# Performance work log

Hardware: AMD Instinct MI355X
Metric: run time of the kernel (lower is better)

Reference implementation:

```python
import jax, jax.numpy as jnp
import numpy as np

B = 32            # decode batch (N flat tokens, q_len=1 each)
D_MODEL = 4096
H = 32            # query heads
HKV = 8           # kv heads (GQA)
HD = 128          # head dim
KVLEN = 2048      # context length per sequence
BLOCK = 256       # paged-cache block size
NBPS = KVLEN // BLOCK          # blocks per sequence = 8
NBLOCKS = B * NBPS             # 256
NSLOTS = NBLOCKS * BLOCK       # 65536
EPS = 1e-6
THETA = 10000.0
NEG = -1e30


def setup_inputs() -> dict:
    key = jax.random.key(0)
    ks = jax.random.split(key, 8)
    seqs = jax.random.normal(ks[0], (B, D_MODEL), dtype=jnp.float32)
    Wq = jax.random.normal(ks[1], (D_MODEL, H * HD), dtype=jnp.float32) * 0.02
    Wk = jax.random.normal(ks[2], (D_MODEL, HKV * HD), dtype=jnp.float32) * 0.02
    Wv = jax.random.normal(ks[3], (D_MODEL, HKV * HD), dtype=jnp.float32) * 0.02
    Wo = jax.random.normal(ks[4], (H * HD, D_MODEL), dtype=jnp.float32) * 0.02
    qn_w = jnp.ones((HD,), dtype=jnp.float32)
    kn_w = jnp.ones((HD,), dtype=jnp.float32)
    k_cache = jax.random.normal(ks[5], (NSLOTS, HKV, HD), dtype=jnp.float32) * 0.02
    v_cache = jax.random.normal(ks[6], (NSLOTS, HKV, HD), dtype=jnp.float32) * 0.02
    # decode step: each seq owns NBPS contiguous blocks; new token goes to last slot
    input_pos = jnp.full((B,), KVLEN - 1, dtype=jnp.int32)
    slot_mapping = (jnp.arange(B, dtype=jnp.int32) * NBPS * BLOCK + (KVLEN - 1)).astype(jnp.int32)
    block_tables = jnp.arange(NBLOCKS, dtype=jnp.int32).reshape(B, NBPS)
    context_lens = jnp.full((B,), KVLEN, dtype=jnp.int32)
    return {
        'seqs': seqs, 'Wq': Wq, 'Wk': Wk, 'Wv': Wv, 'Wo': Wo,
        'qn_w': qn_w, 'kn_w': kn_w, 'k_cache': k_cache, 'v_cache': v_cache,
        'input_pos': input_pos, 'slot_mapping': slot_mapping,
        'block_tables': block_tables, 'context_lens': context_lens,
    }


def _rmsnorm(x, w):
    return x * jax.lax.rsqrt(jnp.mean(x * x, axis=-1, keepdims=True) + EPS) * w


def _rope(x, pos):
    # x: [N, heads, HD], pos: [N]
    half = HD // 2
    inv = 1.0 / (THETA ** (jnp.arange(half, dtype=jnp.float32) / half))
    ang = pos.astype(jnp.float32)[:, None] * inv          # [N, half]
    cos = jnp.cos(ang)[:, None, :]
    sin = jnp.sin(ang)[:, None, :]
    x1, x2 = x[..., :half], x[..., half:]
    return jnp.concatenate([x1 * cos - x2 * sin, x2 * cos + x1 * sin], axis=-1)


def reference(seqs, Wq, Wk, Wv, Wo, qn_w, kn_w, k_cache, v_cache,
              input_pos, slot_mapping, block_tables, context_lens):
    # QKV projections (flat token layout, N = B decode tokens)
    q = (seqs @ Wq).reshape(B, H, HD)
    k = (seqs @ Wk).reshape(B, HKV, HD)
    v = (seqs @ Wv).reshape(B, HKV, HD)
    # qk-norm then RoPE
    q = _rmsnorm(q, qn_w)
    k = _rmsnorm(k, kn_w)
    q = _rope(q, input_pos)
    k = _rope(k, input_pos)
    # paged KV-cache store (slot_mapping scatter)
    kc = k_cache.at[slot_mapping].set(k)
    vc = v_cache.at[slot_mapping].set(v)
    # block-table-indexed gather: slots per sequence [B, KVLEN]
    slots = (block_tables[:, :, None] * BLOCK
             + jnp.arange(BLOCK, dtype=jnp.int32)[None, None, :]).reshape(B, -1)
    K = kc[slots]   # [B, L, HKV, HD]
    V = vc[slots]   # [B, L, HKV, HD]
    L = slots.shape[1]
    # GQA attention: group query heads over kv heads
    G = H // HKV
    qg = q.reshape(B, HKV, G, HD)
    scale = 1.0 / jnp.sqrt(jnp.float32(HD))
    scores = jnp.einsum('bkgd,blkd->bkgl', qg, K) * scale   # [B, HKV, G, L]
    valid = jnp.arange(L, dtype=jnp.int32)[None, :] < context_lens[:, None]
    scores = jnp.where(valid[:, None, None, :], scores, NEG)
    p = jax.nn.softmax(scores, axis=-1)
    out = jnp.einsum('bkgl,blkd->bkgd', p, V).reshape(B, H * HD)
    return out @ Wo
```

## Files before the change

kernel.cpp:

```cpp
#include <hip/hip_runtime.h>
#include <hip/hip_bf16.h>
#include <math.h>

#define B_     32
#define DM_    4096
#define H_     32
#define HKV_   8
#define G_     4
#define HD_    128
#define KVLEN_ 2048
#define NBPS_  8
#define NQKV_  6144
#define KSPLIT_ 16
#define KC_    256
#define ASPLIT_ 16
#define APOS_  128

__global__ __launch_bounds__(256) void qkv_gemm(
    const float* __restrict__ seqs, const float* __restrict__ Wq,
    const float* __restrict__ Wk, const float* __restrict__ Wv,
    float* __restrict__ P1) {
  const int tid = threadIdx.x;
  const int nid = blockIdx.x % 24;
  const int kid = blockIdx.x / 24;
  const int k0 = kid * KC_;

  __shared__ __align__(16) float sT[KC_ * 36];
  #pragma unroll
  for (int m = 0; m < 32; ++m)
    sT[tid * 36 + m] = seqs[m * DM_ + k0 + tid];
  __syncthreads();

  const int ct = tid & 127;
  const int mh = tid >> 7;
  const int n  = nid * 256 + ct * 2;

  const float* W; int col, ldw;
  if (nid < 16)      { W = Wq; col = n;        ldw = 4096; }
  else if (nid < 20) { W = Wk; col = n - 4096; ldw = 1024; }
  else               { W = Wv; col = n - 5120; ldw = 1024; }

  float2 acc[16];
  #pragma unroll
  for (int r = 0; r < 16; ++r) acc[r] = make_float2(0.f, 0.f);

  const float2* wp = (const float2*)(W + (size_t)k0 * ldw + col);
  const int ldw2 = ldw >> 1;

  #pragma unroll 4
  for (int kk = 0; kk < KC_; ++kk) {
    float2 w = wp[(size_t)kk * ldw2];
    const float4* s4 = (const float4*)(sT + kk * 36 + mh * 16);
    #pragma unroll
    for (int rq = 0; rq < 4; ++rq) {
      float4 a = s4[rq];
      acc[rq*4+0].x = fmaf(a.x, w.x, acc[rq*4+0].x);
      acc[rq*4+0].y = fmaf(a.x, w.y, acc[rq*4+0].y);
      acc[rq*4+1].x = fmaf(a.y, w.x, acc[rq*4+1].x);
      acc[rq*4+1].y = fmaf(a.y, w.y, acc[rq*4+1].y);
      acc[rq*4+2].x = fmaf(a.z, w.x, acc[rq*4+2].x);
      acc[rq*4+2].y = fmaf(a.z, w.y, acc[rq*4+2].y);
      acc[rq*4+3].x = fmaf(a.w, w.x, acc[rq*4+3].x);
      acc[rq*4+3].y = fmaf(a.w, w.y, acc[rq*4+3].y);
    }
  }

  float* o = P1 + (size_t)kid * 32 * NQKV_ + n;
  #pragma unroll
  for (int r = 0; r < 16; ++r) {
    int m = mh * 16 + r;
    *(float2*)(o + (size_t)m * NQKV_) = acc[r];
  }
}

__global__ __launch_bounds__(128) void reduce_norm_rope(
    const float* __restrict__ P1, const float* __restrict__ qn_w,
    const float* __restrict__ kn_w, const int* __restrict__ input_pos,
    float* __restrict__ qf, float* __restrict__ knew, float* __restrict__ vnew) {
  const int b = blockIdx.x / 48;
  const int hh = blockIdx.x % 48;
  const int tid = threadIdx.x;

  int col0, kind;
  if (hh < 32)      { kind = 0; col0 = hh * 128; }
  else if (hh < 40) { kind = 1; col0 = 4096 + (hh - 32) * 128; }
  else              { kind = 2; col0 = 5120 + (hh - 40) * 128; }

  float x = 0.f;
  const float* p = P1 + (size_t)b * NQKV_ + col0 + tid;
  #pragma unroll
  for (int s = 0; s < KSPLIT_; ++s) x += p[(size_t)s * 32 * NQKV_];

  if (kind == 2) {
    vnew[(size_t)b * 1024 + (hh - 40) * 128 + tid] = x;
    return;
  }

  __shared__ float lds[128];
  __shared__ float wred[2];
  float ss = x * x;
  #pragma unroll
  for (int off = 32; off > 0; off >>= 1) ss += __shfl_down(ss, off);
  if ((tid & 63) == 0) wred[tid >> 6] = ss;
  __syncthreads();
  float tot = wred[0] + wred[1];
  float r = rsqrtf(tot * (1.f / 128.f) + 1e-6f);
  const float* wv = (kind == 0) ? qn_w : kn_w;
  x = x * r * wv[tid];

  lds[tid] = x;
  __syncthreads();

  if (tid < 64) {
    float pos = (float)input_pos[b];
    float inv = powf(10000.f, -(float)tid * (1.f / 64.f));
    float ang = pos * inv;
    float c = cosf(ang), s = sinf(ang);
    float x1 = lds[tid], x2 = lds[tid + 64];
    float o1 = x1 * c - x2 * s;
    float o2 = x2 * c + x1 * s;
    float* dst = (kind == 0) ? (qf + (size_t)b * 4096 + hh * 128)
                             : (knew + (size_t)b * 1024 + (hh - 32) * 128);
    dst[tid] = o1;
    dst[tid + 64] = o2;
  }
}

__global__ __launch_bounds__(512) void attn_decode(
    const float* __restrict__ qf, const float* __restrict__ knew,
    const float* __restrict__ vnew, const float* __restrict__ kc,
    const float* __restrict__ vc, const int* __restrict__ block_tables,
    const int* __restrict__ slot_mapping, const int* __restrict__ context_lens,
    float* __restrict__ pacc, float* __restrict__ pls) {
  const int b   = blockIdx.x >> 4;
  const int sp  = blockIdx.x & 15;
  const int tid = threadIdx.x;
  const int w   = tid >> 6;
  const int lane = tid & 63;
  const int gi  = lane >> 4;
  const int l16 = lane & 15;
  const int d0  = l16 * 8;

  const int ctx   = context_lens[b];
  const int fslot = slot_mapping[b];
  const int base  = sp * APOS_;

  const int page  = block_tables[b * NBPS_ + (base >> 8)];
  const int slot0 = (page << 8) + (base & 255);

  const float scale = 0.08838834764831845f;
  float q[4][8];
  #pragma unroll
  for (int g = 0; g < 4; ++g) {
    const float4* qp = (const float4*)(qf + ((size_t)b * H_ + w * G_ + g) * HD_ + d0);
    float4 a = qp[0], c = qp[1];
    q[g][0] = a.x * scale; q[g][1] = a.y * scale; q[g][2] = a.z * scale; q[g][3] = a.w * scale;
    q[g][4] = c.x * scale; q[g][5] = c.y * scale; q[g][6] = c.z * scale; q[g][7] = c.w * scale;
  }

  const float* knp = knew + ((size_t)b * HKV_ + w) * HD_ + d0;
  const float* vnp = vnew + ((size_t)b * HKV_ + w) * HD_ + d0;
  const float* kcb = kc + ((size_t)slot0 * HKV_ + w) * HD_ + d0;
  const float* vcb = vc + ((size_t)slot0 * HKV_ + w) * HD_ + d0;

  float ls[4] = {0.f, 0.f, 0.f, 0.f};
  float acc[4][8];
  #pragma unroll
  for (int g = 0; g < 4; ++g)
    #pragma unroll
    for (int j = 0; j < 8; ++j) acc[g][j] = 0.f;

  for (int it = 0; it < APOS_ / 4; ++it) {
    const int off = it * 4 + gi;
    const int pos = base + off;
    if (pos < ctx) {
      const int slot = slot0 + off;
      const float* kp = (slot == fslot) ? knp : (kcb + (size_t)off * (HKV_ * HD_));
      const float* vp = (slot == fslot) ? vnp : (vcb + (size_t)off * (HKV_ * HD_));
      float4 k1 = ((const float4*)kp)[0];
      float4 k2 = ((const float4*)kp)[1];
      float4 v1 = ((const float4*)vp)[0];
      float4 v2 = ((const float4*)vp)[1];
      float kk8[8] = {k1.x, k1.y, k1.z, k1.w, k2.x, k2.y, k2.z, k2.w};
      float vv[8]  = {v1.x, v1.y, v1.z, v1.w, v2.x, v2.y, v2.z, v2.w};

      float s[4];
      #pragma unroll
      for (int g = 0; g < 4; ++g) {
        float t = 0.f;
        #pragma unroll
        for (int j = 0; j < 8; ++j) t = fmaf(q[g][j], kk8[j], t);
        s[g] = t;
      }
      #pragma unroll
      for (int o2 = 1; o2 < 16; o2 <<= 1) {
        #pragma unroll
        for (int g = 0; g < 4; ++g) s[g] += __shfl_xor(s[g], o2);
      }
      #pragma unroll
      for (int g = 0; g < 4; ++g) {
        float pw = __expf(s[g]);
        ls[g] += pw;
        #pragma unroll
        for (int j = 0; j < 8; ++j) acc[g][j] = fmaf(pw, vv[j], acc[g][j]);
      }
    }
  }

  #pragma unroll
  for (int o2 = 16; o2 < 64; o2 <<= 1) {
    #pragma unroll
    for (int g = 0; g < 4; ++g) {
      ls[g] += __shfl_xor(ls[g], o2);
      #pragma unroll
      for (int j = 0; j < 8; ++j) acc[g][j] += __shfl_xor(acc[g][j], o2);
    }
  }

  if (gi == 0) {
    #pragma unroll
    for (int g = 0; g < 4; ++g) {
      float* dst = pacc + (((size_t)sp * B_ + b) * H_ + (w * G_ + g)) * HD_ + d0;
      float4 o1 = {acc[g][0], acc[g][1], acc[g][2], acc[g][3]};
      float4 o2 = {acc[g][4], acc[g][5], acc[g][6], acc[g][7]};
      ((float4*)dst)[0] = o1;
      ((float4*)dst)[1] = o2;
      if (l16 == 0) pls[((size_t)sp * B_ + b) * H_ + (w * G_ + g)] = ls[g];
    }
  }
}

__global__ __launch_bounds__(256) void attn_merge(
    const float* __restrict__ pacc, const float* __restrict__ pls,
    float* __restrict__ attnb) {
  const int idx = blockIdx.x * 256 + threadIdx.x;
  const int bh  = idx >> 5;
  const float4* p4 = (const float4*)pacc;
  float4 A = {0.f, 0.f, 0.f, 0.f};
  float L = 0.f;
  #pragma unroll
  for (int sp = 0; sp < ASPLIT_; ++sp) {
    float4 t = p4[(size_t)sp * 32768 + idx];
    A.x += t.x; A.y += t.y; A.z += t.z; A.w += t.w;
    L += pls[sp * (B_ * H_) + bh];
  }
  float r = 1.f / L;
  A.x *= r; A.y *= r; A.z *= r; A.w *= r;
  ((float4*)attnb)[idx] = A;
}

__global__ __launch_bounds__(256) void oproj_gemm(
    const float* __restrict__ A, const float* __restrict__ Wo,
    float* __restrict__ P2) {
  const int tid = threadIdx.x;
  const int nid = blockIdx.x & 15;
  const int kid = blockIdx.x >> 4;
  const int k0 = kid * KC_;

  __shared__ __align__(16) float sT[KC_ * 36];
  #pragma unroll
  for (int m = 0; m < 32; ++m)
    sT[tid * 36 + m] = A[m * 4096 + k0 + tid];
  __syncthreads();

  const int ct = tid & 127;
  const int mh = tid >> 7;
  const int n  = nid * 256 + ct * 2;

  float2 acc[16];
  #pragma unroll
  for (int r = 0; r < 16; ++r) acc[r] = make_float2(0.f, 0.f);

  const float2* wp = (const float2*)(Wo + (size_t)k0 * 4096 + n);

  #pragma unroll 4
  for (int kk = 0; kk < KC_; ++kk) {
    float2 w = wp[(size_t)kk * 2048];
    const float4* s4 = (const float4*)(sT + kk * 36 + mh * 16);
    #pragma unroll
    for (int rq = 0; rq < 4; ++rq) {
      float4 a = s4[rq];
      acc[rq*4+0].x = fmaf(a.x, w.x, acc[rq*4+0].x);
      acc[rq*4+0].y = fmaf(a.x, w.y, acc[rq*4+0].y);
      acc[rq*4+1].x = fmaf(a.y, w.x, acc[rq*4+1].x);
      acc[rq*4+1].y = fmaf(a.y, w.y, acc[rq*4+1].y);
      acc[rq*4+2].x = fmaf(a.z, w.x, acc[rq*4+2].x);
      acc[rq*4+2].y = fmaf(a.z, w.y, acc[rq*4+2].y);
      acc[rq*4+3].x = fmaf(a.w, w.x, acc[rq*4+3].x);
      acc[rq*4+3].y = fmaf(a.w, w.y, acc[rq*4+3].y);
    }
  }

  float* o = P2 + (size_t)kid * 32 * 4096 + n;
  #pragma unroll
  for (int r = 0; r < 16; ++r) {
    int m = mh * 16 + r;
    *(float2*)(o + (size_t)m * 4096) = acc[r];
  }
}

__global__ __launch_bounds__(256) void oproj_reduce(
    const float* __restrict__ P2, float* __restrict__ out) {
  const int idx = blockIdx.x * 256 + threadIdx.x;
  float s = 0.f;
  #pragma unroll
  for (int t = 0; t < KSPLIT_; ++t) s += P2[(size_t)t * 131072 + idx];
  out[idx] = s;
}

extern "C" void kernel_launch(void* const* d_in, const int* in_sizes, int n_in,
                              void* d_out, int out_size, void* d_ws, size_t ws_size,
                              hipStream_t stream) {
  const float* seqs = (const float*)d_in[0];
  const float* Wq   = (const float*)d_in[1];
  const float* Wk   = (const float*)d_in[2];
  const float* Wv   = (const float*)d_in[3];
  const float* Wo   = (const float*)d_in[4];
  const float* qn_w = (const float*)d_in[5];
  const float* kn_w = (const float*)d_in[6];
  const float* kc   = (const float*)d_in[7];
  const float* vc   = (const float*)d_in[8];
  const int* input_pos = (const int*)d_in[9];
  const int* slot_map  = (const int*)d_in[10];
  const int* btab      = (const int*)d_in[11];
  const int* ctx       = (const int*)d_in[12];
  float* out = (float*)d_out;

  char* w = (char*)d_ws;
  float* P1    = (float*)(w);
  float* qf    = (float*)(w + 12582912);
  float* knew  = (float*)(w + 13107200);
  float* vnew  = (float*)(w + 13238272);
  float* attnb = (float*)(w + 13369344);
  float* pacc  = (float*)(w + 13893632);
  float* pls   = (float*)(w + 22282240);
  float* P2    = (float*)(w + 22347776);

  qkv_gemm<<<24 * KSPLIT_, 256, 0, stream>>>(seqs, Wq, Wk, Wv, P1);
  reduce_norm_rope<<<B_ * 48, 128, 0, stream>>>(P1, qn_w, kn_w, input_pos, qf, knew, vnew);
  attn_decode<<<B_ * ASPLIT_, 512, 0, stream>>>(qf, knew, vnew, kc, vc, btab, slot_map, ctx, pacc, pls);
  attn_merge<<<128, 256, 0, stream>>>(pacc, pls, attnb);
  oproj_gemm<<<16 * KSPLIT_, 256, 0, stream>>>(attnb, Wo, P2);
  oproj_reduce<<<512, 256, 0, stream>>>(P2, out);
}
```

Baseline: 211.8 us.

## Pre-transpose GEMM activations, stream weights nontemporally, add fast path in attention

Adds a small transpose kernel so the QKV and output-projection GEMMs read the activation operand straight from global memory (wave-uniform, cached) instead of staging it through LDS with a barrier. Weight and KV-cache loads become nontemporal, and unrolling is increased. The attention kernel gets a branch-free fast path for splits that hold neither the newly written slot nor a context boundary. The output projection uses 512 threads with 8 rows each to raise occupancy. In exchange it adds two extra kernel launches and workspace for the transposed activations.

```diff
diff --git a/kernel.cpp b/kernel.cpp
--- a/kernel.cpp
+++ b/kernel.cpp
@@ -16,8 +16,30 @@
 #define ASPLIT_ 16
 #define APOS_  128
 
+typedef float vf4 __attribute__((ext_vector_type(4)));
+typedef float vf2 __attribute__((ext_vector_type(2)));
+
+__global__ __launch_bounds__(256) void transpose32(
+    const float* __restrict__ in, float* __restrict__ out) {
+  __shared__ float t[32][65];
+  const int tid = threadIdx.x;
+  const int k0 = blockIdx.x * 64;
+  #pragma unroll
+  for (int it = 0; it < 8; ++it) {
+    int m = it * 4 + (tid >> 6);
+    int k = tid & 63;
+    t[m][k] = in[(size_t)m * DM_ + k0 + k];
+  }
+  __syncthreads();
+  #pragma unroll
+  for (int it = 0; it < 8; ++it) {
+    int flat = it * 256 + tid;
+    out[(size_t)k0 * 32 + flat] = t[flat & 31][flat >> 5];
+  }
+}
+
 __global__ __launch_bounds__(256) void qkv_gemm(
-    const float* __restrict__ seqs, const float* __restrict__ Wq,
+    const float* __restrict__ seqsT, const float* __restrict__ Wq,
     const float* __restrict__ Wk, const float* __restrict__ Wv,
     float* __restrict__ P1) {
   const int tid = threadIdx.x;
@@ -25,14 +47,8 @@
   const int kid = blockIdx.x / 24;
   const int k0 = kid * KC_;
 
-  __shared__ __align__(16) float sT[KC_ * 36];
-  #pragma unroll
-  for (int m = 0; m < 32; ++m)
-    sT[tid * 36 + m] = seqs[m * DM_ + k0 + tid];
-  __syncthreads();
-
   const int ct = tid & 127;
-  const int mh = tid >> 7;
+  const int mh16 = __builtin_amdgcn_readfirstlane((tid >> 7) << 4);
   const int n  = nid * 256 + ct * 2;
 
   const float* W; int col, ldw;
@@ -44,31 +60,30 @@
   #pragma unroll
   for (int r = 0; r < 16; ++r) acc[r] = make_float2(0.f, 0.f);
 
-  const float2* wp = (const float2*)(W + (size_t)k0 * ldw + col);
+  const vf2* wp = (const vf2*)(W + (size_t)k0 * ldw + col);
   const int ldw2 = ldw >> 1;
-
-  #pragma unroll 4
+  const vf4* ap = (const vf4*)(seqsT + (size_t)k0 * 32 + mh16);
+
+  #pragma unroll 8
   for (int kk = 0; kk < KC_; ++kk) {
-    float2 w = wp[(size_t)kk * ldw2];
-    const float4* s4 = (const float4*)(sT + kk * 36 + mh * 16);
-    #pragma unroll
-    for (int rq = 0; rq < 4; ++rq) {
-      float4 a = s4[rq];
-      acc[rq*4+0].x = fmaf(a.x, w.x, acc[rq*4+0].x);
-      acc[rq*4+0].y = fmaf(a.x, w.y, acc[rq*4+0].y);
-      acc[rq*4+1].x = fmaf(a.y, w.x, acc[rq*4+1].x);
-      acc[rq*4+1].y = fmaf(a.y, w.y, acc[rq*4+1].y);
-      acc[rq*4+2].x = fmaf(a.z, w.x, acc[rq*4+2].x);
-      acc[rq*4+2].y = fmaf(a.z, w.y, acc[rq*4+2].y);
-      acc[rq*4+3].x = fmaf(a.w, w.x, acc[rq*4+3].x);
-      acc[rq*4+3].y = fmaf(a.w, w.y, acc[rq*4+3].y);
-    }
+    vf2 w = __builtin_nontemporal_load(wp + (size_t)kk * ldw2);
+    vf4 a0 = ap[kk * 8 + 0];
+    vf4 a1 = ap[kk * 8 + 1];
+    vf4 a2 = ap[kk * 8 + 2];
+    vf4 a3 = ap[kk * 8 + 3];
+    #define FMA2(av, r) \
+      acc[r].x = fmaf(av, w.x, acc[r].x); acc[r].y = fmaf(av, w.y, acc[r].y);
+    FMA2(a0.x, 0)  FMA2(a0.y, 1)  FMA2(a0.z, 2)  FMA2(a0.w, 3)
+    FMA2(a1.x, 4)  FMA2(a1.y, 5)  FMA2(a1.z, 6)  FMA2(a1.w, 7)
+    FMA2(a2.x, 8)  FMA2(a2.y, 9)  FMA2(a2.z, 10) FMA2(a2.w, 11)
+    FMA2(a3.x, 12) FMA2(a3.y, 13) FMA2(a3.z, 14) FMA2(a3.w, 15)
+    #undef FMA2
   }
 
   float* o = P1 + (size_t)kid * 32 * NQKV_ + n;
   #pragma unroll
   for (int r = 0; r < 16; ++r) {
-    int m = mh * 16 + r;
+    int m = mh16 + r;
     *(float2*)(o + (size_t)m * NQKV_) = acc[r];
   }
 }
@@ -147,6 +162,9 @@
 
   const int page  = block_tables[b * NBPS_ + (base >> 8)];
   const int slot0 = (page << 8) + (base & 255);
+  const int rel   = fslot - slot0;
+  const bool hasf = (rel >= 0) && (rel < APOS_);
+  const int nv    = min(APOS_, ctx - base);
 
   const float scale = 0.08838834764831845f;
   float q[4][8];
@@ -170,42 +188,59 @@
     #pragma unroll
     for (int j = 0; j < 8; ++j) acc[g][j] = 0.f;
 
-  for (int it = 0; it < APOS_ / 4; ++it) {
-    const int off = it * 4 + gi;
-    const int pos = base + off;
-    if (pos < ctx) {
-      const int slot = slot0 + off;
-      const float* kp = (slot == fslot) ? knp : (kcb + (size_t)off * (HKV_ * HD_));
-      const float* vp = (slot == fslot) ? vnp : (vcb + (size_t)off * (HKV_ * HD_));
-      float4 k1 = ((const float4*)kp)[0];
-      float4 k2 = ((const float4*)kp)[1];
-      float4 v1 = ((const float4*)vp)[0];
-      float4 v2 = ((const float4*)vp)[1];
-      float kk8[8] = {k1.x, k1.y, k1.z, k1.w, k2.x, k2.y, k2.z, k2.w};
-      float vv[8]  = {v1.x, v1.y, v1.z, v1.w, v2.x, v2.y, v2.z, v2.w};
-
-      float s[4];
-      #pragma unroll
-      for (int g = 0; g < 4; ++g) {
-        float t = 0.f;
-        #pragma unroll
-        for (int j = 0; j < 8; ++j) t = fmaf(q[g][j], kk8[j], t);
-        s[g] = t;
+  #define ATTN_STEP(K1, K2, V1, V2)                                       \
+    {                                                                     \
+      float kk8[8] = {K1.x, K1.y, K1.z, K1.w, K2.x, K2.y, K2.z, K2.w};    \
+      float vv[8]  = {V1.x, V1.y, V1.z, V1.w, V2.x, V2.y, V2.z, V2.w};    \
+      float s[4];                                                         \
+      _Pragma("unroll")                                                   \
+      for (int g = 0; g < 4; ++g) {                                       \
+        float t = 0.f;                                                    \
+        _Pragma("unroll")                                                 \
+        for (int j = 0; j < 8; ++j) t = fmaf(q[g][j], kk8[j], t);         \
+        s[g] = t;                                                         \
+      }                                                                   \
+      _Pragma("unroll")                                                   \
+      for (int o2 = 1; o2 < 16; o2 <<= 1) {                               \
+        _Pragma("unroll")                                                 \
+        for (int g = 0; g < 4; ++g) s[g] += __shfl_xor(s[g], o2);         \
+      }                                                                   \
+      _Pragma("unroll")                                                   \
+      for (int g = 0; g < 4; ++g) {                                       \
+        float pw = __expf(s[g]);                                          \
+        ls[g] += pw;                                                      \
+        _Pragma("unroll")                                                 \
+        for (int j = 0; j < 8; ++j) acc[g][j] = fmaf(pw, vv[j], acc[g][j]); \
+      }                                                                   \
+    }
+
+  if (!hasf && nv == APOS_) {
+    #pragma unroll 2
+    for (int it = 0; it < APOS_ / 4; ++it) {
+      const int off = it * 4 + gi;
+      const vf4* kp4 = (const vf4*)(kcb + (size_t)off * (HKV_ * HD_));
+      const vf4* vp4 = (const vf4*)(vcb + (size_t)off * (HKV_ * HD_));
+      vf4 k1 = __builtin_nontemporal_load(kp4);
+      vf4 k2 = __builtin_nontemporal_load(kp4 + 1);
+      vf4 v1 = __builtin_nontemporal_load(vp4);
+      vf4 v2 = __builtin_nontemporal_load(vp4 + 1);
+      ATTN_STEP(k1, k2, v1, v2)
+    }
+  } else {
+    for (int it = 0; it < APOS_ / 4; ++it) {
+      const int off = it * 4 + gi;
+      if (base + off < ctx) {
+        const float* kp = (off == rel) ? knp : (kcb + (size_t)off * (HKV_ * HD_));
+        const float* vp = (off == rel) ? vnp : (vcb + (size_t)off * (HKV_ * HD_));
+        float4 k1 = ((const float4*)kp)[0];
+        float4 k2 = ((const float4*)kp)[1];
+        float4 v1 = ((const float4*)vp)[0];
+        float4 v2 = ((const float4*)vp)[1];
+        ATTN_STEP(k1, k2, v1, v2)
       }
-      #pragma unroll
-      for (int o2 = 1; o2 < 16; o2 <<= 1) {
-        #pragma unroll
-        for (int g = 0; g < 4; ++g) s[g] += __shfl_xor(s[g], o2);
-      }
-      #pragma unroll
-      for (int g = 0; g < 4; ++g) {
-        float pw = __expf(s[g]);
-        ls[g] += pw;
-        #pragma unroll
-        for (int j = 0; j < 8; ++j) acc[g][j] = fmaf(pw, vv[j], acc[g][j]);
-      }
-    }
-  }
+    }
+  }
+  #undef ATTN_STEP
 
   #pragma unroll
   for (int o2 = 16; o2 < 64; o2 <<= 1) {
@@ -249,52 +284,41 @@
   ((float4*)attnb)[idx] = A;
 }
 
-__global__ __launch_bounds__(256) void oproj_gemm(
-    const float* __restrict__ A, const float* __restrict__ Wo,
+__global__ __launch_bounds__(512) void oproj_gemm(
+    const float* __restrict__ attnT, const float* __restrict__ Wo,
     float* __restrict__ P2) {
   const int tid = threadIdx.x;
   const int nid = blockIdx.x & 15;
   const int kid = blockIdx.x >> 4;
   const int k0 = kid * KC_;
 
-  __shared__ __align__(16) float sT[KC_ * 36];
-  #pragma unroll
-  for (int m = 0; m < 32; ++m)
-    sT[tid * 36 + m] = A[m * 4096 + k0 + tid];
-  __syncthreads();
-
   const int ct = tid & 127;
-  const int mh = tid >> 7;
+  const int mq8 = __builtin_amdgcn_readfirstlane((tid >> 7) << 3);
   const int n  = nid * 256 + ct * 2;
 
-  float2 acc[16];
-  #pragma unroll
-  for (int r = 0; r < 16; ++r) acc[r] = make_float2(0.f, 0.f);
-
-  const float2* wp = (const float2*)(Wo + (size_t)k0 * 4096 + n);
-
-  #pragma unroll 4
+  float2 acc[8];
+  #pragma unroll
+  for (int r = 0; r < 8; ++r) acc[r] = make_float2(0.f, 0.f);
+
+  const vf2* wp = (const vf2*)(Wo + (size_t)k0 * 4096 + n);
+  const vf4* ap = (const vf4*)(attnT + (size_t)k0 * 32 + mq8);
+
+  #pragma unroll 8
   for (int kk = 0; kk < KC_; ++kk) {
-    float2 w = wp[(size_t)kk * 2048];
-    const float4* s4 = (const float4*)(sT + kk * 36 + mh * 16);
-    #pragma unroll
-    for (int rq = 0; rq < 4; ++rq) {
-      float4 a = s4[rq];
-      acc[rq*4+0].x = fmaf(a.x, w.x, acc[rq*4+0].x);
-      acc[rq*4+0].y = fmaf(a.x, w.y, acc[rq*4+0].y);
-      acc[rq*4+1].x = fmaf(a.y, w.x, acc[rq*4+1].x);
-      acc[rq*4+1].y = fmaf(a.y, w.y, acc[rq*4+1].y);
-      acc[rq*4+2].x = fmaf(a.z, w.x, acc[rq*4+2].x);
-      acc[rq*4+2].y = fmaf(a.z, w.y, acc[rq*4+2].y);
-      acc[rq*4+3].x = fmaf(a.w, w.x, acc[rq*4+3].x);
-      acc[rq*4+3].y = fmaf(a.w, w.y, acc[rq*4+3].y);
-    }
+    vf2 w = __builtin_nontemporal_load(wp + (size_t)kk * 2048);
+    vf4 a0 = ap[kk * 8 + 0];
+    vf4 a1 = ap[kk * 8 + 1];
+    #define FMA2(av, r) \
+      acc[r].x = fmaf(av, w.x, acc[r].x); acc[r].y = fmaf(av, w.y, acc[r].y);
+    FMA2(a0.x, 0) FMA2(a0.y, 1) FMA2(a0.z, 2) FMA2(a0.w, 3)
+    FMA2(a1.x, 4) FMA2(a1.y, 5) FMA2(a1.z, 6) FMA2(a1.w, 7)
+    #undef FMA2
   }
 
   float* o = P2 + (size_t)kid * 32 * 4096 + n;
   #pragma unroll
-  for (int r = 0; r < 16; ++r) {
-    int m = mh * 16 + r;
+  for (int r = 0; r < 8; ++r) {
+    int m = mq8 + r;
     *(float2*)(o + (size_t)m * 4096) = acc[r];
   }
 }
@@ -327,19 +351,23 @@
   float* out = (float*)d_out;
 
   char* w = (char*)d_ws;
-  float* P1    = (float*)(w);
-  float* qf    = (float*)(w + 12582912);
-  float* knew  = (float*)(w + 13107200);
-  float* vnew  = (float*)(w + 13238272);
-  float* attnb = (float*)(w + 13369344);
-  float* pacc  = (float*)(w + 13893632);
-  float* pls   = (float*)(w + 22282240);
-  float* P2    = (float*)(w + 22347776);
-
-  qkv_gemm<<<24 * KSPLIT_, 256, 0, stream>>>(seqs, Wq, Wk, Wv, P1);
+  float* seqsT = (float*)(w);
+  float* P1    = (float*)(w + 1048576);
+  float* qf    = (float*)(w + 14680064);
+  float* knew  = (float*)(w + 15204352);
+  float* vnew  = (float*)(w + 15335424);
+  float* attnb = (float*)(w + 15466496);
+  float* attnT = (float*)(w + 15990784);
+  float* pacc  = (float*)(w + 16515072);
+  float* pls   = (float*)(w + 24903680);
+  float* P2    = (float*)(w + 24969216);
+
+  transpose32<<<64, 256, 0, stream>>>(seqs, seqsT);
+  qkv_gemm<<<24 * KSPLIT_, 256, 0, stream>>>(seqsT, Wq, Wk, Wv, P1);
   reduce_norm_rope<<<B_ * 48, 128, 0, stream>>>(P1, qn_w, kn_w, input_pos, qf, knew, vnew);
   attn_decode<<<B_ * ASPLIT_, 512, 0, stream>>>(qf, knew, vnew, kc, vc, btab, slot_map, ctx, pacc, pls);
   attn_merge<<<128, 256, 0, stream>>>(pacc, pls, attnb);
-  oproj_gemm<<<16 * KSPLIT_, 256, 0, stream>>>(attnb, Wo, P2);
+  transpose32<<<64, 256, 0, stream>>>(attnb, attnT);
+  oproj_gemm<<<16 * KSPLIT_, 512, 0, stream>>>(attnT, Wo, P2);
   oproj_reduce<<<512, 256, 0, stream>>>(P2, out);
 }
```

Measured after the change: 205.0 us. 1.03x faster.
